# Optimization experiments

Measured on AMD Instinct MI355X. Metric: run time of the kernel, lower is better.

The kernel has to match this reference:

```python
import jax, jax.numpy as jnp
import numpy as np

H = 256
L = 5
N = 50000


def setup_inputs() -> dict:
    key = jax.random.key(0)
    ks = jax.random.split(key, 12)
    E = 800000
    x = jax.random.normal(ks[0], (N, H), dtype=jnp.float32)
    edge_index = jax.random.randint(ks[1], (2, E), 0, N, dtype=jnp.int64)
    edge_weight = jax.random.uniform(ks[2], (E,), dtype=jnp.float32)
    s = 1.0 / np.sqrt(H)
    weight = jax.random.uniform(ks[3], (L, H, H), dtype=jnp.float32, minval=-s, maxval=s)
    w_ih = jax.random.uniform(ks[4], (3 * H, H), dtype=jnp.float32, minval=-s, maxval=s)
    w_hh = jax.random.uniform(ks[5], (3 * H, H), dtype=jnp.float32, minval=-s, maxval=s)
    b_ih = jax.random.uniform(ks[6], (3 * H,), dtype=jnp.float32, minval=-s, maxval=s)
    b_hh = jax.random.uniform(ks[7], (3 * H,), dtype=jnp.float32, minval=-s, maxval=s)
    fc_w = jax.random.uniform(ks[8], (1, H), dtype=jnp.float32, minval=-s, maxval=s)
    fc_b = jax.random.uniform(ks[9], (1,), dtype=jnp.float32, minval=-s, maxval=s)
    return {"x": x, "edge_index": edge_index, "edge_weight": edge_weight,
            "weight": weight, "w_ih": w_ih, "w_hh": w_hh, "b_ih": b_ih,
            "b_hh": b_hh, "fc_w": fc_w, "fc_b": fc_b, "prob": 0}


def _gru_cell(m, h, w_ih, w_hh, b_ih, b_hh):
    # PyTorch GRUCell: gates ordered (r, z, n)
    gi = m @ w_ih.T + b_ih  # [N, 3H]
    gh = h @ w_hh.T + b_hh  # [N, 3H]
    r = jax.nn.sigmoid(gi[:, :H] + gh[:, :H])
    z = jax.nn.sigmoid(gi[:, H:2 * H] + gh[:, H:2 * H])
    n = jnp.tanh(gi[:, 2 * H:] + r * gh[:, 2 * H:])
    return (1.0 - z) * n + z * h


def reference(x, edge_index, edge_weight, weight, w_ih, w_hh, b_ih, b_hh, fc_w, fc_b, prob):
    src = edge_index[0]
    dst = edge_index[1]
    h = x
    for i in range(L):
        m = h @ weight[i]                       # [N, H] per-layer linear transform
        msg = edge_weight[:, None] * m[src]     # [E, H] gather + edge weighting
        agg = jax.ops.segment_sum(msg, dst, num_segments=N)  # scatter-add
        h = _gru_cell(agg, h, w_ih, w_hh, b_ih, b_hh)
    h = jax.nn.relu(h)
    # dropout with p=prob; reference runs deterministically with p=0 (eval mode)
    out = h @ fc_w.T + fc_b                     # [N, 1]
    return out
```

## Files before the change

### kernel.cpp

```cpp
#include <hip/hip_runtime.h>
#include <hip/hip_bf16.h>
#include <math.h>


#define HDIM 256

using bf16x8 = __attribute__((ext_vector_type(8))) short;
using f32x4  = __attribute__((ext_vector_type(4))) float;

__device__ __forceinline__ bf16x8 ldfrag(const ushort* p) {
    union { uint4 u; bf16x8 f; } x;
    x.u = *(const uint4*)p;
    return x.f;
}
#define MFMA(a, b, c) __builtin_amdgcn_mfma_f32_16x16x32_bf16((a), (b), (c), 0, 0, 0)
#define GLD16(g, l)                                                            \
    __builtin_amdgcn_global_load_lds(                                          \
        (const __attribute__((address_space(1))) void*)(g),                    \
        (__attribute__((address_space(3))) void*)(l), 16, 0, 0)

__device__ __forceinline__ float ldf(const void* p, size_t i, int isbf) {
    if (isbf) return __bfloat162float(((const __hip_bfloat16*)p)[i]);
    return ((const float*)p)[i];
}
__device__ __forceinline__ ushort f2bs(float v) {
    __hip_bfloat16 b = __float2bfloat16(v);
    return *(ushort*)&b;
}
__device__ __forceinline__ float bs2f(ushort u) {
    __hip_bfloat16 b = *(__hip_bfloat16*)&u;
    return __bfloat162float(b);
}
__device__ __forceinline__ size_t taddrH(int n, int k) {
    return (size_t)(n >> 4) * 4096 + (size_t)((k >> 5) << 9)
         + (size_t)(((k >> 3) & 3) << 7) + (size_t)((n & 15) << 3) + (k & 7);
}
__device__ __forceinline__ size_t taddrA(int n, int k) {
    return (size_t)(n >> 4) * 8192 + (size_t)((k >> 5) << 9)
         + (size_t)(((k >> 3) & 3) << 7) + (size_t)((n & 15) << 3) + (k & 7);
}

__global__ void detect_k(const void* x, const void* ei, int* flags) {
    if (blockIdx.x == 0 && threadIdx.x == 0) {
        const __hip_bfloat16* xb = (const __hip_bfloat16*)x;
        int isbf = 1;
        for (int i = 0; i < 1024; ++i) {
            float v = fabsf(__bfloat162float(xb[i]));
            if (!(v < 1e6f)) { isbf = 0; break; }
        }
        flags[0] = isbf;
        const int* e32 = (const int*)ei;
        int orv = e32[1] | e32[3] | e32[5] | e32[7] | e32[9] | e32[11];
        flags[1] = (orv == 0) ? 1 : 0;
    }
}

__global__ void conv_h0_k(const void* x, ushort* HH, ushort* HL,
                          const int* flags, int useHL, int Nn, size_t npad256) {
    size_t i = (size_t)blockIdx.x * blockDim.x + threadIdx.x;
    if (i >= npad256) return;
    const int n = (int)(i >> 8), k = (int)(i & 255);
    float v = 0.f;
    if (n < Nn) v = ldf(x, i, flags[0]);
    const ushort hi = f2bs(v);
    const size_t a = taddrH(n, k);
    HH[a] = hi;
    if (useHL) HL[a] = f2bs(v - bs2f(hi));
}

__global__ void prep_k(const void* w, const void* wih, const void* whh,
                       const void* bih, const void* bhh,
                       ushort* BgH, ushort* BgL, ushort* BwH, ushort* BwL,
                       float* bsum, float* bni, float* bnh,
                       const int* flags, int L) {
    int i = blockIdx.x * blockDim.x + threadIdx.x;
    int isbf = flags[0];
    if (i < 1048576) {
        const int j = i >> 10, k = i & 1023;
        const int g = (j >> 4) & 3, b = ((j >> 6) << 4) + (j & 15);
        const int kk = k & 255, seg = k >> 8;
        float v = 0.f;
        if (g == 0) v = (seg < 2) ? ldf(wih, (size_t)b * 256 + kk, isbf)
                                  : ldf(whh, (size_t)b * 256 + kk, isbf);
        else if (g == 1) v = (seg < 2) ? ldf(wih, (size_t)(256 + b) * 256 + kk, isbf)
                                       : ldf(whh, (size_t)(256 + b) * 256 + kk, isbf);
        else if (g == 2) v = (seg < 2) ? ldf(wih, (size_t)(512 + b) * 256 + kk, isbf) : 0.f;
        else             v = (seg < 2) ? 0.f : ldf(whh, (size_t)(512 + b) * 256 + kk, isbf);
        const ushort hi = f2bs(v);
        const int ct = j >> 4, c = k >> 5;
        const size_t a = (size_t)(ct * 32 + c) * 512
                       + (size_t)(((k >> 3) & 3) << 7) + ((j & 15) << 3) + (k & 7);
        BgH[a] = hi; BgL[a] = f2bs(v - bs2f(hi));
    }
    if (i < L * 131072) {
        const int l = i >> 17, r2 = i & 131071;
        const int j = r2 >> 9, k = r2 & 511;
        const int kk = k & 255;
        const float v = ldf(w, ((size_t)l << 16) + (size_t)kk * 256 + j, isbf);
        const ushort hi = f2bs(v);
        const int ct = j >> 4, c = k >> 5;
        const size_t a = (size_t)l * 131072 + (size_t)(ct * 16 + c) * 512
                       + (size_t)(((k >> 3) & 3) << 7) + ((j & 15) << 3) + (k & 7);
        BwH[a] = hi; BwL[a] = f2bs(v - bs2f(hi));
    }
    if (i < 512) bsum[i] = ldf(bih, i, isbf) + ldf(bhh, i, isbf);
    if (i < 256) {
        bni[i] = ldf(bih, 512 + i, isbf);
        bnh[i] = ldf(bhh, 512 + i, isbf);
    }
}


__global__ void zero_int_k(int* p, int n) {
    int i = blockIdx.x * blockDim.x + threadIdx.x;
    if (i < n) p[i] = 0;
}

__global__ void count_k(const void* ei, int* cnt, const int* flags, int E) {
    int e = blockIdx.x * blockDim.x + threadIdx.x;
    if (e >= E) return;
    const int* e32 = (const int*)ei;
    int d = flags[1] ? e32[2 * ((size_t)E + e)] : e32[(size_t)E + e];
    atomicAdd(&cnt[d], 1);
}

__global__ __launch_bounds__(256)
void scan1_k(const int* cnt, int* ptr, int* bsumN, int N) {
    __shared__ int s[256];
    const int t = threadIdx.x;
    const int gid = blockIdx.x * 256 + t;
    int v = (gid < N) ? cnt[gid] : 0;
    const int own = v;
    s[t] = v;
    __syncthreads();
#pragma unroll
    for (int off = 1; off < 256; off <<= 1) {
        int add = (t >= off) ? s[t - off] : 0;
        __syncthreads();
        s[t] += add;
        __syncthreads();
    }
    if (gid < N) ptr[gid] = s[t] - own;
    if (t == 255) bsumN[blockIdx.x] = s[255];
}

__global__ __launch_bounds__(256)
void scan2_k(int* bsumN, int NB) {
    __shared__ int s[256];
    __shared__ int carry;
    const int t = threadIdx.x;
    if (t == 0) carry = 0;
    __syncthreads();
    for (int base = 0; base < NB; base += 256) {
        const int i = base + t;
        int v = (i < NB) ? bsumN[i] : 0;
        const int own = v;
        s[t] = v;
        __syncthreads();
#pragma unroll
        for (int off = 1; off < 256; off <<= 1) {
            int add = (t >= off) ? s[t - off] : 0;
            __syncthreads();
            s[t] += add;
            __syncthreads();
        }
        if (i < NB) bsumN[i] = carry + s[t] - own;
        __syncthreads();
        if (t == 0) carry += s[255];
        __syncthreads();
    }
}

__global__ void scan3_k(int* ptr, int* cursor, const int* bsumN, int N, int E) {
    const int gid = blockIdx.x * 256 + threadIdx.x;
    if (gid < N) {
        const int p = ptr[gid] + bsumN[blockIdx.x];
        ptr[gid] = p;
        cursor[gid] = p;
    }
    if (gid == 0) ptr[N] = E;
}

__global__ void fill_k(const void* ei, const void* ew, int* cursor,
                       int* srcs, float* wse, const int* flags, int E) {
    int e = blockIdx.x * blockDim.x + threadIdx.x;
    if (e >= E) return;
    const int* e32 = (const int*)ei;
    int s, d;
    if (flags[1]) { s = e32[2 * (size_t)e]; d = e32[2 * ((size_t)E + e)]; }
    else          { s = e32[e];             d = e32[(size_t)E + e]; }
    const int p = atomicAdd(&cursor[d], 1);
    srcs[p] = s;
    wse[p] = ldf(ew, e, flags[0]);
}

__global__ __launch_bounds__(256)
void spmm_k(const float* __restrict__ m, const int* __restrict__ ptr,
            const int* __restrict__ srcs, const float* __restrict__ wse,
            ushort* __restrict__ AGG, int N) {
    const int node = blockIdx.x * 4 + (threadIdx.x >> 6);
    if (node >= N) return;
    const int lane4 = (threadIdx.x & 63) << 2;
    const int p0 = ptr[node], p1 = ptr[node + 1];
    float4 acc = make_float4(0.f, 0.f, 0.f, 0.f);
    int j = p0;
    for (; j + 1 < p1; j += 2) {
        const int s0 = srcs[j], s1 = srcs[j + 1];
        const float w0 = wse[j], w1 = wse[j + 1];
        const float4 v0 = *(const float4*)&m[(size_t)s0 * HDIM + lane4];
        const float4 v1 = *(const float4*)&m[(size_t)s1 * HDIM + lane4];
        acc.x = fmaf(w0, v0.x, acc.x); acc.y = fmaf(w0, v0.y, acc.y);
        acc.z = fmaf(w0, v0.z, acc.z); acc.w = fmaf(w0, v0.w, acc.w);
        acc.x = fmaf(w1, v1.x, acc.x); acc.y = fmaf(w1, v1.y, acc.y);
        acc.z = fmaf(w1, v1.z, acc.z); acc.w = fmaf(w1, v1.w, acc.w);
    }
    if (j < p1) {
        const int s0 = srcs[j];
        const float w0 = wse[j];
        const float4 v0 = *(const float4*)&m[(size_t)s0 * HDIM + lane4];
        acc.x = fmaf(w0, v0.x, acc.x); acc.y = fmaf(w0, v0.y, acc.y);
        acc.z = fmaf(w0, v0.z, acc.z); acc.w = fmaf(w0, v0.w, acc.w);
    }
    ushort4 hi, lo;
    hi.x = f2bs(acc.x); lo.x = f2bs(acc.x - bs2f(hi.x));
    hi.y = f2bs(acc.y); lo.y = f2bs(acc.y - bs2f(hi.y));
    hi.z = f2bs(acc.z); lo.z = f2bs(acc.z - bs2f(hi.z));
    hi.w = f2bs(acc.w); lo.w = f2bs(acc.w - bs2f(hi.w));
    *(ushort4*)&AGG[taddrA(node, lane4)] = hi;
    *(ushort4*)&AGG[taddrA(node, 256 + lane4)] = lo;
}

__global__ __launch_bounds__(256)
void m_gemm_k(const ushort* __restrict__ HH, const ushort* __restrict__ HL,
              const ushort* __restrict__ BwHl, const ushort* __restrict__ BwLl,
              float* __restrict__ m, const int* __restrict__ flags,
              int useHL, int nRB) {
    __shared__ ushort lds[12288];
    const int rb = blockIdx.x >> 1, cgB = blockIdx.x & 1;
    if (rb >= nRB) return;
    const int tid = threadIdx.x, lane = tid & 63;
    const int wv = __builtin_amdgcn_readfirstlane(tid >> 6);
    const int wr = wv & 1, wc = wv >> 1;
    const int lm = lane & 15, lq = lane >> 4;
    const int fullsplit = !flags[0];
    const int NCH = useHL ? 16 : 8;
    const int rt = rb * 8, t0 = 2 * wv;
    f32x4 acc[4][4];
#pragma unroll
    for (int i = 0; i < 4; ++i)
#pragma unroll
        for (int j = 0; j < 4; ++j) acc[i][j] = (f32x4){0.f, 0.f, 0.f, 0.f};

    for (int c = 0; c < NCH; ++c) {
        __syncthreads();
        const ushort* a0 = (c < 8)
            ? HH + (size_t)(rt + t0) * 4096 + (size_t)c * 512
            : HL + (size_t)(rt + t0) * 4096 + (size_t)(c - 8) * 512;
        GLD16(a0 + (size_t)lane * 8, &lds[t0 * 512]);
        GLD16(a0 + 4096 + (size_t)lane * 8, &lds[t0 * 512 + 512]);
        const size_t bb = ((size_t)(8 * cgB + t0) * 16 + c) * 512;
        GLD16(BwHl + bb + (size_t)lane * 8, &lds[4096 + t0 * 512]);
        GLD16(BwHl + bb + 8192 + (size_t)lane * 8, &lds[4096 + t0 * 512 + 512]);
        if (fullsplit) {
            GLD16(BwLl + bb + (size_t)lane * 8, &lds[8192 + t0 * 512]);
            GLD16(BwLl + bb + 8192 + (size_t)lane * 8, &lds[8192 + t0 * 512 + 512]);
        }
        __syncthreads();
        bf16x8 af[4], bf[4];
#pragma unroll
        for (int i = 0; i < 4; ++i)
            af[i] = ldfrag(&lds[(4 * wr + i) * 512 + lq * 128 + lm * 8]);
#pragma unroll
        for (int j = 0; j < 4; ++j)
            bf[j] = ldfrag(&lds[4096 + (4 * wc + j) * 512 + lq * 128 + lm * 8]);
#pragma unroll
        for (int i = 0; i < 4; ++i)
#pragma unroll
            for (int j = 0; j < 4; ++j) acc[i][j] = MFMA(af[i], bf[j], acc[i][j]);
        if (fullsplit) {
#pragma unroll
            for (int j = 0; j < 4; ++j) {
                const bf16x8 bl = ldfrag(&lds[8192 + (4 * wc + j) * 512 + lq * 128 + lm * 8]);
#pragma unroll
                for (int i = 0; i < 4; ++i) acc[i][j] = MFMA(af[i], bl, acc[i][j]);
            }
        }
    }
#pragma unroll
    for (int i = 0; i < 4; ++i) {
        const int row = rb * 128 + wr * 64 + i * 16 + lq * 4;
#pragma unroll
        for (int j = 0; j < 4; ++j) {
            const int col = cgB * 128 + wc * 64 + j * 16 + lm;
#pragma unroll
            for (int v = 0; v < 4; ++v)
                m[(size_t)(row + v) * 256 + col] = acc[i][j][v];
        }
    }
}

__global__ __launch_bounds__(256)
void gates_k(const ushort* __restrict__ AGG,
             const ushort* __restrict__ HH, const ushort* __restrict__ HL,
             const ushort* __restrict__ BgH, const ushort* __restrict__ BgL,
             const float* __restrict__ bsum, const float* __restrict__ bni,
             const float* __restrict__ bnh,
             ushort* __restrict__ HnH, ushort* __restrict__ HnL,
             const int* __restrict__ flags, int useHL, int nRB) {
    __shared__ ushort lds[12288];
    const int x = blockIdx.x & 7, rem = blockIdx.x >> 3;
    const int cgB = rem & 7, rbHi = rem >> 3;
    const int rb = rbHi * 8 + x;
    if (rb >= nRB) return;
    const int tid = threadIdx.x, lane = tid & 63;
    const int wv = __builtin_amdgcn_readfirstlane(tid >> 6);
    const int wr = wv & 1, wc = wv >> 1;
    const int lm = lane & 15, lq = lane >> 4;
    const int fullsplit = !flags[0];
    const int NCH = useHL ? 32 : 24;
    const int rt = rb * 8, t0 = 2 * wv;
    f32x4 acc[4][4];
#pragma unroll
    for (int i = 0; i < 4; ++i)
#pragma unroll
        for (int j = 0; j < 4; ++j) acc[i][j] = (f32x4){0.f, 0.f, 0.f, 0.f};

    for (int c = 0; c < NCH; ++c) {
        __syncthreads();
        const ushort* a0;
        size_t stride;
        if (c < 16)      { a0 = AGG + (size_t)(rt + t0) * 8192 + (size_t)c * 512; stride = 8192; }
        else if (c < 24) { a0 = HH + (size_t)(rt + t0) * 4096 + (size_t)(c - 16) * 512; stride = 4096; }
        else             { a0 = HL + (size_t)(rt + t0) * 4096 + (size_t)(c - 24) * 512; stride = 4096; }
        GLD16(a0 + (size_t)lane * 8, &lds[t0 * 512]);
        GLD16(a0 + stride + (size_t)lane * 8, &lds[t0 * 512 + 512]);
        const size_t bb = ((size_t)(8 * cgB + t0) * 32 + c) * 512;
        GLD16(BgH + bb + (size_t)lane * 8, &lds[4096 + t0 * 512]);
        GLD16(BgH + bb + 16384 + (size_t)lane * 8, &lds[4096 + t0 * 512 + 512]);
        if (fullsplit) {
            GLD16(BgL + bb + (size_t)lane * 8, &lds[8192 + t0 * 512]);
            GLD16(BgL + bb + 16384 + (size_t)lane * 8, &lds[8192 + t0 * 512 + 512]);
        }
        __syncthreads();
        bf16x8 af[4], bf[4];
#pragma unroll
        for (int i = 0; i < 4; ++i)
            af[i] = ldfrag(&lds[(4 * wr + i) * 512 + lq * 128 + lm * 8]);
#pragma unroll
        for (int j = 0; j < 4; ++j)
            bf[j] = ldfrag(&lds[4096 + (4 * wc + j) * 512 + lq * 128 + lm * 8]);
#pragma unroll
        for (int i = 0; i < 4; ++i)
#pragma unroll
            for (int j = 0; j < 4; ++j) acc[i][j] = MFMA(af[i], bf[j], acc[i][j]);
        if (fullsplit) {
#pragma unroll
            for (int j = 0; j < 4; ++j) {
                const bf16x8 bl = ldfrag(&lds[8192 + (4 * wc + j) * 512 + lq * 128 + lm * 8]);
#pragma unroll
                for (int i = 0; i < 4; ++i) acc[i][j] = MFMA(af[i], bl, acc[i][j]);
            }
        }
    }
    const int b = (2 * cgB + wc) * 16 + lm;
    const float rbias = bsum[b], zbias = bsum[256 + b];
    const float ibias = bni[b], hbias = bnh[b];
#pragma unroll
    for (int i = 0; i < 4; ++i) {
        const int row0 = rb * 128 + wr * 64 + i * 16 + lq * 4;
#pragma unroll
        for (int v = 0; v < 4; ++v) {
            const int row = row0 + v;
            const size_t ho = taddrH(row, b);
            float hold = bs2f(HH[ho]);
            if (useHL) hold += bs2f(HL[ho]);
            const float r = 1.f / (1.f + expf(-(acc[i][0][v] + rbias)));
            const float z = 1.f / (1.f + expf(-(acc[i][1][v] + zbias)));
            const float nn = tanhf(acc[i][2][v] + ibias + r * (acc[i][3][v] + hbias));
            const float hv = (1.f - z) * nn + z * hold;
            const ushort hi = f2bs(hv);
            HnH[ho] = hi;
            if (useHL) HnL[ho] = f2bs(hv - bs2f(hi));
        }
    }
}

__global__ void final_k(const ushort* __restrict__ HH, const ushort* __restrict__ HL,
                        const void* fcw, const void* fcb,
                        void* out, const int* flags, int useHL, int N) {
    const int n = blockIdx.x;
    const int t = threadIdx.x;
    const int isbf = flags[0];
    const size_t off = taddrH(n, t);
    float h = bs2f(HH[off]);
    if (useHL) h += bs2f(HL[off]);
    float v = fmaxf(h, 0.f) * ldf(fcw, t, isbf);
#pragma unroll
    for (int offx = 32; offx >= 1; offx >>= 1) v += __shfl_down(v, offx);
    __shared__ float red[4];
    if ((t & 63) == 0) red[t >> 6] = v;
    __syncthreads();
    if (t == 0) {
        const float s = red[0] + red[1] + red[2] + red[3] + ldf(fcb, 0, isbf);
        if (isbf) ((__hip_bfloat16*)out)[n] = __float2bfloat16(s);
        else      ((float*)out)[n] = s;
    }
}

extern "C" void kernel_launch(void* const* d_in, const int* in_sizes, int n_in,
                              void* d_out, int out_size, void* d_ws, size_t ws_size,
                              hipStream_t stream) {
    const int H = HDIM;
    const int N = in_sizes[0] / H;
    const int E = in_sizes[2];
    const int L = in_sizes[3] / (H * H);
    const int NB = (N + 255) / 256;
    const int nRB = (N + 127) / 128;
    const size_t NPAD = (size_t)nRB * 128;
    const size_t hHalf = NPAD * 256;
    const size_t aggHalf = NPAD * 512;

    char* p = (char*)d_ws;
    int*    flags = (int*)p;              p += 64;
    ushort* AGG  = (ushort*)p;            p += aggHalf * 2;
    ushort* HxH  = (ushort*)p;            p += hHalf * 2;
    ushort* HyH  = (ushort*)p;            p += hHalf * 2;
    float*  m    = (float*)p;             p += NPAD * 256 * 4;
    ushort* BgH  = (ushort*)p;            p += (size_t)1048576 * 2;
    ushort* BgL  = (ushort*)p;            p += (size_t)1048576 * 2;
    ushort* BwH  = (ushort*)p;            p += (size_t)L * 131072 * 2;
    ushort* BwL  = (ushort*)p;            p += (size_t)L * 131072 * 2;
    float*  bsum = (float*)p;             p += 512 * 4;
    float*  bni  = (float*)p;             p += 256 * 4;
    float*  bnh  = (float*)p;             p += 256 * 4;
    int*    ptr  = (int*)p;               p += (size_t)(N + 1) * 4;
    int*    cursor = (int*)p;             p += (size_t)N * 4;
    int*    bsumN  = (int*)p;             p += (size_t)NB * 4;
    int*    srcs   = (int*)p;             p += (size_t)E * 4;
    float*  wse    = (float*)p;           p += (size_t)E * 4;
    const size_t need_reduced = (size_t)(p - (char*)d_ws);
    ushort* HxL = (ushort*)p;
    ushort* HyL = (ushort*)(p + hHalf * 2);
    const size_t need_full = need_reduced + 2 * hHalf * 2;
    const int useHL = (ws_size >= need_full) ? 1 : 0;
    if (!useHL) { HxL = HxH; HyL = HyH; }

    detect_k<<<dim3(1), dim3(64), 0, stream>>>(d_in[0], d_in[1], flags);
    conv_h0_k<<<dim3((unsigned)NPAD), dim3(256), 0, stream>>>(
        d_in[0], HxH, HxL, flags, useHL, N, NPAD * 256);
    prep_k<<<dim3(4096), dim3(256), 0, stream>>>(
        d_in[3], d_in[4], d_in[5], d_in[6], d_in[7],
        BgH, BgL, BwH, BwL, bsum, bni, bnh, flags, L);

    zero_int_k<<<dim3(NB), dim3(256), 0, stream>>>(cursor, N);
    count_k<<<dim3((E + 255) / 256), dim3(256), 0, stream>>>(d_in[1], cursor, flags, E);
    scan1_k<<<dim3(NB), dim3(256), 0, stream>>>(cursor, ptr, bsumN, N);
    scan2_k<<<dim3(1), dim3(256), 0, stream>>>(bsumN, NB);
    scan3_k<<<dim3(NB), dim3(256), 0, stream>>>(ptr, cursor, bsumN, N, E);
    fill_k<<<dim3((E + 255) / 256), dim3(256), 0, stream>>>(
        d_in[1], d_in[2], cursor, srcs, wse, flags, E);

    const dim3 blk(256);
    const unsigned gGrid = 64u * (unsigned)((nRB + 7) / 8);
    ushort *HcH = HxH, *HcL = HxL, *HnH = HyH, *HnL = HyL;
    for (int l = 0; l < L; ++l) {
        m_gemm_k<<<dim3((unsigned)(2 * nRB)), blk, 0, stream>>>(
            HcH, HcL, BwH + (size_t)l * 131072, BwL + (size_t)l * 131072,
            m, flags, useHL, nRB);
        spmm_k<<<dim3((N + 3) / 4), blk, 0, stream>>>(m, ptr, srcs, wse, AGG, N);
        gates_k<<<dim3(gGrid), blk, 0, stream>>>(
            AGG, HcH, HcL, BgH, BgL, bsum, bni, bnh, HnH, HnL, flags, useHL, nRB);
        ushort* t;
        t = HcH; HcH = HnH; HnH = t;
        t = HcL; HcL = HnL; HnL = t;
    }
    final_k<<<dim3(N), blk, 0, stream>>>(
        HcH, HcL, d_in[8], d_in[9], d_out, flags, useHL, N);
}
```

Measured before the change: 2.286 ms.

## Double-buffer LDS staging and skip zero gate blocks and low-weight terms in GEMMs

Both GEMM kernels now use two LDS buffers and prefetch the next K-chunk while the current one is computed, leaving one barrier per iteration. MFMA sections are wrapped in s_setprio. The gates kernel skips loading and multiplying the weight sub-blocks that are structurally zero: the h-gate column block for agg chunks and the i-gate block for h chunks. Both kernels also drop the low-part weight correction for the HL chunks (a lo*lo term). This doubles LDS use per block, which may reduce occupancy, and slightly changes precision.

```diff
diff --git a/kernel.cpp b/kernel.cpp
--- a/kernel.cpp
+++ b/kernel.cpp
@@ -235,7 +235,7 @@
               const ushort* __restrict__ BwHl, const ushort* __restrict__ BwLl,
               float* __restrict__ m, const int* __restrict__ flags,
               int useHL, int nRB) {
-    __shared__ ushort lds[12288];
+    __shared__ ushort lds[24576];
     const int rb = blockIdx.x >> 1, cgB = blockIdx.x & 1;
     if (rb >= nRB) return;
     const int tid = threadIdx.x, lane = tid & 63;
@@ -251,41 +251,51 @@
 #pragma unroll
         for (int j = 0; j < 4; ++j) acc[i][j] = (f32x4){0.f, 0.f, 0.f, 0.f};
 
-    for (int c = 0; c < NCH; ++c) {
-        __syncthreads();
+    auto stage = [&](int c, int sb) {
+        const int lb = sb * 12288;
         const ushort* a0 = (c < 8)
             ? HH + (size_t)(rt + t0) * 4096 + (size_t)c * 512
             : HL + (size_t)(rt + t0) * 4096 + (size_t)(c - 8) * 512;
-        GLD16(a0 + (size_t)lane * 8, &lds[t0 * 512]);
-        GLD16(a0 + 4096 + (size_t)lane * 8, &lds[t0 * 512 + 512]);
-        const size_t bb = ((size_t)(8 * cgB + t0) * 16 + c) * 512;
-        GLD16(BwHl + bb + (size_t)lane * 8, &lds[4096 + t0 * 512]);
-        GLD16(BwHl + bb + 8192 + (size_t)lane * 8, &lds[4096 + t0 * 512 + 512]);
-        if (fullsplit) {
-            GLD16(BwLl + bb + (size_t)lane * 8, &lds[8192 + t0 * 512]);
-            GLD16(BwLl + bb + 8192 + (size_t)lane * 8, &lds[8192 + t0 * 512 + 512]);
-        }
-        __syncthreads();
-        bf16x8 af[4], bf[4];
+        GLD16(a0 + (size_t)lane * 8, &lds[lb + t0 * 512]);
+        GLD16(a0 + 4096 + (size_t)lane * 8, &lds[lb + t0 * 512 + 512]);
+        const size_t bb = ((size_t)(8 * cgB + t0) * 16 + (size_t)c) * 512;
+        GLD16(BwHl + bb + (size_t)lane * 8, &lds[lb + 4096 + t0 * 512]);
+        GLD16(BwHl + bb + 8192 + (size_t)lane * 8, &lds[lb + 4096 + t0 * 512 + 512]);
+        if (fullsplit && c < 8) {
+            GLD16(BwLl + bb + (size_t)lane * 8, &lds[lb + 8192 + t0 * 512]);
+            GLD16(BwLl + bb + 8192 + (size_t)lane * 8, &lds[lb + 8192 + t0 * 512 + 512]);
+        }
+    };
+
+    stage(0, 0);
+    __syncthreads();
+    for (int c = 0; c < NCH; ++c) {
+        if (c + 1 < NCH) stage(c + 1, (c + 1) & 1);
+        const int lb = (c & 1) * 12288;
+        const int dolo = fullsplit && c < 8;
+        bf16x8 af[4];
 #pragma unroll
         for (int i = 0; i < 4; ++i)
-            af[i] = ldfrag(&lds[(4 * wr + i) * 512 + lq * 128 + lm * 8]);
-#pragma unroll
-        for (int j = 0; j < 4; ++j)
-            bf[j] = ldfrag(&lds[4096 + (4 * wc + j) * 512 + lq * 128 + lm * 8]);
-#pragma unroll
-        for (int i = 0; i < 4; ++i)
-#pragma unroll
-            for (int j = 0; j < 4; ++j) acc[i][j] = MFMA(af[i], bf[j], acc[i][j]);
-        if (fullsplit) {
+            af[i] = ldfrag(&lds[lb + (4 * wr + i) * 512 + lq * 128 + lm * 8]);
+        __builtin_amdgcn_s_setprio(1);
+#pragma unroll
+        for (int j = 0; j < 4; ++j) {
+            const bf16x8 bj = ldfrag(&lds[lb + 4096 + (4 * wc + j) * 512 + lq * 128 + lm * 8]);
+#pragma unroll
+            for (int i = 0; i < 4; ++i) acc[i][j] = MFMA(af[i], bj, acc[i][j]);
+        }
+        if (dolo) {
 #pragma unroll
             for (int j = 0; j < 4; ++j) {
-                const bf16x8 bl = ldfrag(&lds[8192 + (4 * wc + j) * 512 + lq * 128 + lm * 8]);
+                const bf16x8 bl = ldfrag(&lds[lb + 8192 + (4 * wc + j) * 512 + lq * 128 + lm * 8]);
 #pragma unroll
                 for (int i = 0; i < 4; ++i) acc[i][j] = MFMA(af[i], bl, acc[i][j]);
             }
         }
-    }
+        __builtin_amdgcn_s_setprio(0);
+        __syncthreads();
+    }
+
 #pragma unroll
     for (int i = 0; i < 4; ++i) {
         const int row = rb * 128 + wr * 64 + i * 16 + lq * 4;
@@ -307,7 +317,7 @@
              const float* __restrict__ bnh,
              ushort* __restrict__ HnH, ushort* __restrict__ HnL,
              const int* __restrict__ flags, int useHL, int nRB) {
-    __shared__ ushort lds[12288];
+    __shared__ ushort lds[24576];
     const int x = blockIdx.x & 7, rem = blockIdx.x >> 3;
     const int cgB = rem & 7, rbHi = rem >> 3;
     const int rb = rbHi * 8 + x;
@@ -325,43 +335,62 @@
 #pragma unroll
         for (int j = 0; j < 4; ++j) acc[i][j] = (f32x4){0.f, 0.f, 0.f, 0.f};
 
+    auto stage = [&](int c, int sb) {
+        const int lb = sb * 12288;
+        const ushort* a0;
+        size_t astride;
+        if (c < 16)      { a0 = AGG + (size_t)(rt + t0) * 8192 + (size_t)c * 512; astride = 8192; }
+        else if (c < 24) { a0 = HH + (size_t)(rt + t0) * 4096 + (size_t)(c - 16) * 512; astride = 4096; }
+        else             { a0 = HL + (size_t)(rt + t0) * 4096 + (size_t)(c - 24) * 512; astride = 4096; }
+        GLD16(a0 + (size_t)lane * 8, &lds[lb + t0 * 512]);
+        GLD16(a0 + astride + (size_t)lane * 8, &lds[lb + t0 * 512 + 512]);
+        const int jskip = (c < 16) ? 3 : 2;
+        const size_t bb = ((size_t)(8 * cgB + t0) * 32 + (size_t)c) * 512;
+        if ((t0 & 3) != jskip)
+            GLD16(BgH + bb + (size_t)lane * 8, &lds[lb + 4096 + t0 * 512]);
+        if (((t0 + 1) & 3) != jskip)
+            GLD16(BgH + bb + 16384 + (size_t)lane * 8, &lds[lb + 4096 + t0 * 512 + 512]);
+        const int dolo = fullsplit && (c < 8 || (c >= 16 && c < 24));
+        if (dolo) {
+            if ((t0 & 3) != jskip)
+                GLD16(BgL + bb + (size_t)lane * 8, &lds[lb + 8192 + t0 * 512]);
+            if (((t0 + 1) & 3) != jskip)
+                GLD16(BgL + bb + 16384 + (size_t)lane * 8, &lds[lb + 8192 + t0 * 512 + 512]);
+        }
+    };
+
+    stage(0, 0);
+    __syncthreads();
     for (int c = 0; c < NCH; ++c) {
-        __syncthreads();
-        const ushort* a0;
-        size_t stride;
-        if (c < 16)      { a0 = AGG + (size_t)(rt + t0) * 8192 + (size_t)c * 512; stride = 8192; }
-        else if (c < 24) { a0 = HH + (size_t)(rt + t0) * 4096 + (size_t)(c - 16) * 512; stride = 4096; }
-        else             { a0 = HL + (size_t)(rt + t0) * 4096 + (size_t)(c - 24) * 512; stride = 4096; }
-        GLD16(a0 + (size_t)lane * 8, &lds[t0 * 512]);
-        GLD16(a0 + stride + (size_t)lane * 8, &lds[t0 * 512 + 512]);
-        const size_t bb = ((size_t)(8 * cgB + t0) * 32 + c) * 512;
-        GLD16(BgH + bb + (size_t)lane * 8, &lds[4096 + t0 * 512]);
-        GLD16(BgH + bb + 16384 + (size_t)lane * 8, &lds[4096 + t0 * 512 + 512]);
-        if (fullsplit) {
-            GLD16(BgL + bb + (size_t)lane * 8, &lds[8192 + t0 * 512]);
-            GLD16(BgL + bb + 16384 + (size_t)lane * 8, &lds[8192 + t0 * 512 + 512]);
-        }
-        __syncthreads();
-        bf16x8 af[4], bf[4];
+        if (c + 1 < NCH) stage(c + 1, (c + 1) & 1);
+        const int lb = (c & 1) * 12288;
+        const int jskip = (c < 16) ? 3 : 2;
+        const int dolo = fullsplit && (c < 8 || (c >= 16 && c < 24));
+        bf16x8 af[4];
 #pragma unroll
         for (int i = 0; i < 4; ++i)
-            af[i] = ldfrag(&lds[(4 * wr + i) * 512 + lq * 128 + lm * 8]);
-#pragma unroll
-        for (int j = 0; j < 4; ++j)
-            bf[j] = ldfrag(&lds[4096 + (4 * wc + j) * 512 + lq * 128 + lm * 8]);
-#pragma unroll
-        for (int i = 0; i < 4; ++i)
-#pragma unroll
-            for (int j = 0; j < 4; ++j) acc[i][j] = MFMA(af[i], bf[j], acc[i][j]);
-        if (fullsplit) {
+            af[i] = ldfrag(&lds[lb + (4 * wr + i) * 512 + lq * 128 + lm * 8]);
+        __builtin_amdgcn_s_setprio(1);
+#pragma unroll
+        for (int j = 0; j < 4; ++j) {
+            if (j == jskip) continue;
+            const bf16x8 bj = ldfrag(&lds[lb + 4096 + (4 * wc + j) * 512 + lq * 128 + lm * 8]);
+#pragma unroll
+            for (int i = 0; i < 4; ++i) acc[i][j] = MFMA(af[i], bj, acc[i][j]);
+        }
+        if (dolo) {
 #pragma unroll
             for (int j = 0; j < 4; ++j) {
-                const bf16x8 bl = ldfrag(&lds[8192 + (4 * wc + j) * 512 + lq * 128 + lm * 8]);
+                if (j == jskip) continue;
+                const bf16x8 bl = ldfrag(&lds[lb + 8192 + (4 * wc + j) * 512 + lq * 128 + lm * 8]);
 #pragma unroll
                 for (int i = 0; i < 4; ++i) acc[i][j] = MFMA(af[i], bl, acc[i][j]);
             }
         }
-    }
+        __builtin_amdgcn_s_setprio(0);
+        __syncthreads();
+    }
+
     const int b = (2 * cgB + wc) * 16 + lm;
     const float rbias = bsum[b], zbias = bsum[256 + b];
     const float ibias = bni[b], hbias = bnh[b];
```

After: 2.115 ms. -7.5%, faster.
